# Performance work log

Hardware: AMD Instinct MI355X
Metric: run time of the kernel (lower is better)

## Reference

```python
import jax, jax.numpy as jnp
import numpy as np

BETA = 1.0
NUM_CLASSES = 64  # upper bound on region ids per image (mask.max()+1 in original)


def setup_inputs() -> dict:
    key = jax.random.key(0)
    k1, k2, k3 = jax.random.split(key, 3)
    B, C, H, W = 16, 3, 512, 512
    inp = jax.random.normal(k1, (B, C, H, W), dtype=jnp.float32)
    tgt = jax.random.normal(k2, (B, C, H, W), dtype=jnp.float32)
    mask = jax.random.randint(k3, (B, H, W), 0, NUM_CLASSES, dtype=jnp.int32)
    return {"input": inp, "target": tgt, "mask": mask}


def reference(input, target, mask):
    B, C, H, W = input.shape
    # per-element L1 (reduce=False)
    loss = jnp.abs(input - target)                      # [B,C,H,W]
    w = jax.lax.stop_gradient(loss)                     # detached copy
    # segmented mean over (channels x region pixels) per (batch, class)
    seg = (jnp.arange(B, dtype=mask.dtype)[:, None, None] * NUM_CLASSES + mask).reshape(-1)  # [B*H*W]
    w_csum = w.sum(axis=1).reshape(-1)                  # sum over channels per pixel, [B*H*W]
    sums = jax.ops.segment_sum(w_csum, seg, num_segments=B * NUM_CLASSES)
    cnts = jax.ops.segment_sum(jnp.ones_like(w_csum), seg, num_segments=B * NUM_CLASSES)
    avg = sums / jnp.maximum(cnts * C, 1.0)             # mean over C*area elements; safe for empty regions
    # broadcast region averages back (same value across channels)
    weight = avg[seg].reshape(B, 1, H, W)               # [B,1,H,W]
    weight = weight / jnp.max(weight)
    weight = jnp.clip(weight, 0.0, 1.0)
    return jnp.mean(loss * (weight * BETA + 1.0))
```

## Files before the change

### kernel.cpp

```cpp
#include <hip/hip_runtime.h>
#include <hip/hip_bf16.h>

#define NUM_CLASSES 64
#define BATCH 16
#define CHAN 3
#define HW (512 * 512)
#define BPB 64
#define THREADS 256
#define NREP 4

__global__ __launch_bounds__(THREADS) void frl_accum(
    const float4* __restrict__ inp,
    const float4* __restrict__ tgt,
    const int4* __restrict__ mask,
    float* __restrict__ g_sum,
    unsigned int* __restrict__ g_cnt)
{
    __shared__ float s_sum[NREP][NUM_CLASSES];
    __shared__ unsigned int s_cnt[NREP][NUM_CLASSES];
    const int t = threadIdx.x;
    for (int i = t; i < NREP * NUM_CLASSES; i += THREADS) {
        ((float*)s_sum)[i] = 0.0f;
        ((unsigned int*)s_cnt)[i] = 0u;
    }
    __syncthreads();

    const int b   = blockIdx.x / BPB;
    const int blk = blockIdx.x % BPB;
    const int PPB = HW / BPB;
    const int GPB = PPB / 4;
    const int rep = t & (NREP - 1);

    const int g0    = blk * GPB;
    const int cbase = b * (CHAN * HW / 4);
    const int mbase = b * (HW / 4);

    for (int g = t; g < GPB; g += THREADS) {
        const int4 m4 = mask[mbase + g0 + g];
        float l[4] = {0.f, 0.f, 0.f, 0.f};
        #pragma unroll
        for (int c = 0; c < CHAN; ++c) {
            const int idx = cbase + c * (HW / 4) + g0 + g;
            const float4 a = inp[idx];
            const float4 v = tgt[idx];
            l[0] += fabsf(a.x - v.x);
            l[1] += fabsf(a.y - v.y);
            l[2] += fabsf(a.z - v.z);
            l[3] += fabsf(a.w - v.w);
        }
        atomicAdd(&s_sum[rep][m4.x], l[0]);
        atomicAdd(&s_sum[rep][m4.y], l[1]);
        atomicAdd(&s_sum[rep][m4.z], l[2]);
        atomicAdd(&s_sum[rep][m4.w], l[3]);
        atomicAdd(&s_cnt[rep][m4.x], 1u);
        atomicAdd(&s_cnt[rep][m4.y], 1u);
        atomicAdd(&s_cnt[rep][m4.z], 1u);
        atomicAdd(&s_cnt[rep][m4.w], 1u);
    }
    __syncthreads();
    if (t < NUM_CLASSES) {
        float fs = 0.0f;
        unsigned int cs = 0u;
        #pragma unroll
        for (int r = 0; r < NREP; ++r) { fs += s_sum[r][t]; cs += s_cnt[r][t]; }
        atomicAdd(&g_sum[b * NUM_CLASSES + t], fs);
        atomicAdd(&g_cnt[b * NUM_CLASSES + t], cs);
    }
}

__global__ __launch_bounds__(256) void frl_finalize(
    const float* __restrict__ g_sum,
    const unsigned int* __restrict__ g_cnt,
    float* __restrict__ out)
{
    const int NSEG = BATCH * NUM_CLASSES;
    __shared__ float s_avg[BATCH * NUM_CLASSES];
    __shared__ float red[256];
    const int t = threadIdx.x;

    float lmax = 0.0f;
    for (int s = t; s < NSEG; s += 256) {
        const float sum = g_sum[s];
        const float cnt = (float)g_cnt[s];
        const float avg = sum / fmaxf(cnt * (float)CHAN, 1.0f);
        s_avg[s] = avg;
        lmax = fmaxf(lmax, avg);
    }
    red[t] = lmax;
    __syncthreads();
    for (int off = 128; off > 0; off >>= 1) {
        if (t < off) red[t] = fmaxf(red[t], red[t + off]);
        __syncthreads();
    }
    const float maxavg = fmaxf(red[0], 1e-30f);
    __syncthreads();

    float part = 0.0f;
    for (int s = t; s < NSEG; s += 256) {
        const float w = fminf(fmaxf(s_avg[s] / maxavg, 0.0f), 1.0f);
        part += g_sum[s] * (1.0f + w);
    }
    red[t] = part;
    __syncthreads();
    for (int off = 128; off > 0; off >>= 1) {
        if (t < off) red[t] += red[t + off];
        __syncthreads();
    }
    if (t == 0) {
        out[0] = red[0] / (float)((size_t)BATCH * CHAN * HW);
    }
}

extern "C" void kernel_launch(void* const* d_in, const int* in_sizes, int n_in,
                              void* d_out, int out_size, void* d_ws, size_t ws_size,
                              hipStream_t stream) {
    const float4* inp = (const float4*)d_in[0];
    const float4* tgt = (const float4*)d_in[1];
    const int4* mask  = (const int4*)d_in[2];

    float* g_sum        = (float*)d_ws;
    unsigned int* g_cnt = (unsigned int*)((char*)d_ws + BATCH * NUM_CLASSES * sizeof(float));

    hipMemsetAsync(d_ws, 0, 2 * BATCH * NUM_CLASSES * sizeof(float), stream);
    frl_accum<<<BATCH * BPB, THREADS, 0, stream>>>(inp, tgt, mask, g_sum, g_cnt);
    frl_finalize<<<1, 256, 0, stream>>>(g_sum, g_cnt, (float*)d_out);
}
```

Baseline: 142.9 us.

## Double-buffer global loads in accumulation loop and pad shared histograms

Replaces the strided per-thread loop with a fixed four-iteration unrolled loop that software-prefetches the next iteration's mask, input and target vectors into registers while the current ones are reduced. The first loads are issued before the shared-memory histogram is zeroed, so that latency overlaps the initialisation and barrier. The shared replica arrays get padding to reduce bank conflicts, and launch bounds request two blocks per SM. The aim is to hide memory latency in this bandwidth-bound pass. The cost is higher register pressure, and the fixed NITER assumes GPB equals NITER times THREADS.

```diff
diff --git a/kernel.cpp b/kernel.cpp
--- a/kernel.cpp
+++ b/kernel.cpp
@@ -7,56 +7,86 @@
 #define HW (512 * 512)
 #define BPB 64
 #define THREADS 256
+#define NITER 4
 #define NREP 4
+#define CPAD 8
 
-__global__ __launch_bounds__(THREADS) void frl_accum(
+__global__ __launch_bounds__(THREADS, 2) void frl_accum(
     const float4* __restrict__ inp,
     const float4* __restrict__ tgt,
     const int4* __restrict__ mask,
     float* __restrict__ g_sum,
     unsigned int* __restrict__ g_cnt)
 {
-    __shared__ float s_sum[NREP][NUM_CLASSES];
-    __shared__ unsigned int s_cnt[NREP][NUM_CLASSES];
+    __shared__ float s_sum[NREP][NUM_CLASSES + CPAD];
+    __shared__ unsigned int s_cnt[NREP][NUM_CLASSES + CPAD];
     const int t = threadIdx.x;
-    for (int i = t; i < NREP * NUM_CLASSES; i += THREADS) {
+
+    const int b   = blockIdx.x / BPB;
+    const int blk = blockIdx.x % BPB;
+    const int GPB = HW / 4 / BPB;
+    const int rep = t & (NREP - 1);
+
+    const int g0    = blk * GPB;
+    const int CS    = HW / 4;
+    const int cbase = b * (CHAN * CS) + g0 + t;
+    const int mbase = b * CS + g0 + t;
+
+    int4   ms[2];
+    float4 ai[2][CHAN];
+    float4 at[2][CHAN];
+
+    ms[0]    = mask[mbase];
+    ai[0][0] = inp[cbase + 0 * CS];
+    ai[0][1] = inp[cbase + 1 * CS];
+    ai[0][2] = inp[cbase + 2 * CS];
+    at[0][0] = tgt[cbase + 0 * CS];
+    at[0][1] = tgt[cbase + 1 * CS];
+    at[0][2] = tgt[cbase + 2 * CS];
+
+    for (int i = t; i < NREP * (NUM_CLASSES + CPAD); i += THREADS) {
         ((float*)s_sum)[i] = 0.0f;
         ((unsigned int*)s_cnt)[i] = 0u;
     }
     __syncthreads();
 
-    const int b   = blockIdx.x / BPB;
-    const int blk = blockIdx.x % BPB;
-    const int PPB = HW / BPB;
-    const int GPB = PPB / 4;
-    const int rep = t & (NREP - 1);
+    #pragma unroll
+    for (int it = 0; it < NITER; ++it) {
+        const int cur = it & 1;
+        const int nxt = cur ^ 1;
+        if (it < NITER - 1) {
+            const int off = (it + 1) * THREADS;
+            ms[nxt]    = mask[mbase + off];
+            ai[nxt][0] = inp[cbase + 0 * CS + off];
+            ai[nxt][1] = inp[cbase + 1 * CS + off];
+            ai[nxt][2] = inp[cbase + 2 * CS + off];
+            at[nxt][0] = tgt[cbase + 0 * CS + off];
+            at[nxt][1] = tgt[cbase + 1 * CS + off];
+            at[nxt][2] = tgt[cbase + 2 * CS + off];
+        }
+        const float l0 = fabsf(ai[cur][0].x - at[cur][0].x)
+                       + fabsf(ai[cur][1].x - at[cur][1].x)
+                       + fabsf(ai[cur][2].x - at[cur][2].x);
+        const float l1 = fabsf(ai[cur][0].y - at[cur][0].y)
+                       + fabsf(ai[cur][1].y - at[cur][1].y)
+                       + fabsf(ai[cur][2].y - at[cur][2].y);
+        const float l2 = fabsf(ai[cur][0].z - at[cur][0].z)
+                       + fabsf(ai[cur][1].z - at[cur][1].z)
+                       + fabsf(ai[cur][2].z - at[cur][2].z);
+        const float l3 = fabsf(ai[cur][0].w - at[cur][0].w)
+                       + fabsf(ai[cur][1].w - at[cur][1].w)
+                       + fabsf(ai[cur][2].w - at[cur][2].w);
+        const int4 m = ms[cur];
+        atomicAdd(&s_sum[rep][m.x], l0);
+        atomicAdd(&s_sum[rep][m.y], l1);
+        atomicAdd(&s_sum[rep][m.z], l2);
+        atomicAdd(&s_sum[rep][m.w], l3);
+        atomicAdd(&s_cnt[rep][m.x], 1u);
+        atomicAdd(&s_cnt[rep][m.y], 1u);
+        atomicAdd(&s_cnt[rep][m.z], 1u);
+        atomicAdd(&s_cnt[rep][m.w], 1u);
+    }
 
-    const int g0    = blk * GPB;
-    const int cbase = b * (CHAN * HW / 4);
-    const int mbase = b * (HW / 4);
-
-    for (int g = t; g < GPB; g += THREADS) {
-        const int4 m4 = mask[mbase + g0 + g];
-        float l[4] = {0.f, 0.f, 0.f, 0.f};
-        #pragma unroll
-        for (int c = 0; c < CHAN; ++c) {
-            const int idx = cbase + c * (HW / 4) + g0 + g;
-            const float4 a = inp[idx];
-            const float4 v = tgt[idx];
-            l[0] += fabsf(a.x - v.x);
-            l[1] += fabsf(a.y - v.y);
-            l[2] += fabsf(a.z - v.z);
-            l[3] += fabsf(a.w - v.w);
-        }
-        atomicAdd(&s_sum[rep][m4.x], l[0]);
-        atomicAdd(&s_sum[rep][m4.y], l[1]);
-        atomicAdd(&s_sum[rep][m4.z], l[2]);
-        atomicAdd(&s_sum[rep][m4.w], l[3]);
-        atomicAdd(&s_cnt[rep][m4.x], 1u);
-        atomicAdd(&s_cnt[rep][m4.y], 1u);
-        atomicAdd(&s_cnt[rep][m4.z], 1u);
-        atomicAdd(&s_cnt[rep][m4.w], 1u);
-    }
     __syncthreads();
     if (t < NUM_CLASSES) {
         float fs = 0.0f;
```

Result: no change. 143.0 us (+0.0%).

## Double-buffer inputs via direct global-to-LDS async loads in accumulation kernel

Applied to the files above, without the earlier changes.

Replaces direct per-thread global float4 loads with global_load_lds async copies into a double-buffered LDS staging area per wavefront. The next chunk's loads are issued before the current chunk is processed, using manual vmcnt waits, to overlap memory latency with the compute and atomic work. It also pads the shared histogram arrays. This relies on the 16-byte LDS-direct load support and correct wait counts, and adds LDS usage that may reduce occupancy.

```diff
diff --git a/kernel.cpp b/kernel.cpp
--- a/kernel.cpp
+++ b/kernel.cpp
@@ -7,56 +7,100 @@
 #define HW (512 * 512)
 #define BPB 64
 #define THREADS 256
+#define WAVES 4
+#define PXW 256
+#define CHUNK (PXW * WAVES)
+#define NCHUNK 4
 #define NREP 4
+#define CPAD 8
+#define SLOTS 7
+
+#define WAITCNT_VM7 0xF77
+#define WAITCNT_VM0 0xF70
+
+typedef __attribute__((address_space(3))) void* lds_vp;
+typedef const __attribute__((address_space(1))) void* gm_vp;
 
 __global__ __launch_bounds__(THREADS) void frl_accum(
-    const float4* __restrict__ inp,
-    const float4* __restrict__ tgt,
-    const int4* __restrict__ mask,
+    const float* __restrict__ inp,
+    const float* __restrict__ tgt,
+    const int*   __restrict__ mask,
     float* __restrict__ g_sum,
     unsigned int* __restrict__ g_cnt)
 {
-    __shared__ float s_sum[NREP][NUM_CLASSES];
-    __shared__ unsigned int s_cnt[NREP][NUM_CLASSES];
-    const int t = threadIdx.x;
-    for (int i = t; i < NREP * NUM_CLASSES; i += THREADS) {
+    __shared__ float lds[2][WAVES][SLOTS * PXW];
+    __shared__ float s_sum[NREP][NUM_CLASSES + CPAD];
+    __shared__ unsigned int s_cnt[NREP][NUM_CLASSES + CPAD];
+
+    const int t   = threadIdx.x;
+    const int w   = t >> 6;
+    const int l   = t & 63;
+    const int b   = blockIdx.x / BPB;
+    const int blk = blockIdx.x % BPB;
+    const int rep = t & (NREP - 1);
+
+    const float* inb = inp  + (size_t)b * CHAN * HW;
+    const float* tgb = tgt  + (size_t)b * CHAN * HW;
+    const int*   mkb = mask + (size_t)b * HW;
+
+    auto stage = [&](int buf, int i) {
+        const int px0 = blk * (CHUNK * NCHUNK) + i * CHUNK + w * PXW;
+        float* ldsw = &lds[buf][w][0];
+        #pragma unroll
+        for (int c = 0; c < CHAN; ++c) {
+            __builtin_amdgcn_global_load_lds(
+                (gm_vp)(inb + c * HW + px0 + l * 4),
+                (lds_vp)(ldsw + c * PXW), 16, 0, 0);
+            __builtin_amdgcn_global_load_lds(
+                (gm_vp)(tgb + c * HW + px0 + l * 4),
+                (lds_vp)(ldsw + (3 + c) * PXW), 16, 0, 0);
+        }
+        __builtin_amdgcn_global_load_lds(
+            (gm_vp)(mkb + px0 + l * 4),
+            (lds_vp)(ldsw + 6 * PXW), 16, 0, 0);
+    };
+
+    stage(0, 0);
+
+    for (int i = t; i < NREP * (NUM_CLASSES + CPAD); i += THREADS) {
         ((float*)s_sum)[i] = 0.0f;
         ((unsigned int*)s_cnt)[i] = 0u;
     }
     __syncthreads();
 
-    const int b   = blockIdx.x / BPB;
-    const int blk = blockIdx.x % BPB;
-    const int PPB = HW / BPB;
-    const int GPB = PPB / 4;
-    const int rep = t & (NREP - 1);
+    #pragma unroll
+    for (int i = 0; i < NCHUNK; ++i) {
+        const int buf = i & 1;
+        if (i + 1 < NCHUNK) {
+            stage(buf ^ 1, i + 1);
+            __builtin_amdgcn_s_waitcnt(WAITCNT_VM7);
+        } else {
+            __builtin_amdgcn_s_waitcnt(WAITCNT_VM0);
+        }
+        const float* ldsw = &lds[buf][w][0];
+        const float4 a0 = *(const float4*)(ldsw + 0 * PXW + l * 4);
+        const float4 a1 = *(const float4*)(ldsw + 1 * PXW + l * 4);
+        const float4 a2 = *(const float4*)(ldsw + 2 * PXW + l * 4);
+        const float4 b0 = *(const float4*)(ldsw + 3 * PXW + l * 4);
+        const float4 b1 = *(const float4*)(ldsw + 4 * PXW + l * 4);
+        const float4 b2 = *(const float4*)(ldsw + 5 * PXW + l * 4);
+        const int4   m  = *(const int4*)  (ldsw + 6 * PXW + l * 4);
 
-    const int g0    = blk * GPB;
-    const int cbase = b * (CHAN * HW / 4);
-    const int mbase = b * (HW / 4);
+        const float l0 = fabsf(a0.x - b0.x) + fabsf(a1.x - b1.x) + fabsf(a2.x - b2.x);
+        const float l1 = fabsf(a0.y - b0.y) + fabsf(a1.y - b1.y) + fabsf(a2.y - b2.y);
+        const float l2 = fabsf(a0.z - b0.z) + fabsf(a1.z - b1.z) + fabsf(a2.z - b2.z);
+        const float l3 = fabsf(a0.w - b0.w) + fabsf(a1.w - b1.w) + fabsf(a2.w - b2.w);
 
-    for (int g = t; g < GPB; g += THREADS) {
-        const int4 m4 = mask[mbase + g0 + g];
-        float l[4] = {0.f, 0.f, 0.f, 0.f};
-        #pragma unroll
-        for (int c = 0; c < CHAN; ++c) {
-            const int idx = cbase + c * (HW / 4) + g0 + g;
-            const float4 a = inp[idx];
-            const float4 v = tgt[idx];
-            l[0] += fabsf(a.x - v.x);
-            l[1] += fabsf(a.y - v.y);
-            l[2] += fabsf(a.z - v.z);
-            l[3] += fabsf(a.w - v.w);
-        }
-        atomicAdd(&s_sum[rep][m4.x], l[0]);
-        atomicAdd(&s_sum[rep][m4.y], l[1]);
-        atomicAdd(&s_sum[rep][m4.z], l[2]);
-        atomicAdd(&s_sum[rep][m4.w], l[3]);
-        atomicAdd(&s_cnt[rep][m4.x], 1u);
-        atomicAdd(&s_cnt[rep][m4.y], 1u);
-        atomicAdd(&s_cnt[rep][m4.z], 1u);
-        atomicAdd(&s_cnt[rep][m4.w], 1u);
+        atomicAdd(&s_sum[rep][m.x], l0);
+        atomicAdd(&s_sum[rep][m.y], l1);
+        atomicAdd(&s_sum[rep][m.z], l2);
+        atomicAdd(&s_sum[rep][m.w], l3);
+        atomicAdd(&s_cnt[rep][m.x], 1u);
+        atomicAdd(&s_cnt[rep][m.y], 1u);
+        atomicAdd(&s_cnt[rep][m.z], 1u);
+        atomicAdd(&s_cnt[rep][m.w], 1u);
     }
+
     __syncthreads();
     if (t < NUM_CLASSES) {
         float fs = 0.0f;
@@ -114,9 +158,9 @@
 extern "C" void kernel_launch(void* const* d_in, const int* in_sizes, int n_in,
                               void* d_out, int out_size, void* d_ws, size_t ws_size,
                               hipStream_t stream) {
-    const float4* inp = (const float4*)d_in[0];
-    const float4* tgt = (const float4*)d_in[1];
-    const int4* mask  = (const int4*)d_in[2];
+    const float* inp = (const float*)d_in[0];
+    const float* tgt = (const float*)d_in[1];
+    const int* mask  = (const int*)d_in[2];
 
     float* g_sum        = (float*)d_ws;
     unsigned int* g_cnt = (unsigned int*)((char*)d_ws + BATCH * NUM_CLASSES * sizeof(float));
```

Result: slower. 147.0 us (+2.8%).

## Split accumulation across channels per block with nontemporal loads and full unroll

Applied to the files above, without the earlier changes.

The grid grows from batch×slab blocks to channel×batch×slab blocks. Each block now handles one channel of one slab, and only the channel-0 blocks update the counts. Input and target are read with nontemporal loads, the pixel loop is fully unrolled, and the shared histograms are padded. In exchange, the mask is reread three times, and the shared atomic adds for sums triple because per-pixel channel sums are no longer formed in registers.

```diff
diff --git a/kernel.cpp b/kernel.cpp
--- a/kernel.cpp
+++ b/kernel.cpp
@@ -5,66 +5,72 @@
 #define BATCH 16
 #define CHAN 3
 #define HW (512 * 512)
-#define BPB 64
+#define SLABS 64
+#define SLABPX (HW / SLABS)
 #define THREADS 256
 #define NREP 4
+#define CPAD 8
+
+typedef float  fx4 __attribute__((ext_vector_type(4)));
+typedef int    ix4 __attribute__((ext_vector_type(4)));
 
 __global__ __launch_bounds__(THREADS) void frl_accum(
-    const float4* __restrict__ inp,
-    const float4* __restrict__ tgt,
-    const int4* __restrict__ mask,
+    const fx4* __restrict__ inp,
+    const fx4* __restrict__ tgt,
+    const ix4* __restrict__ mask,
     float* __restrict__ g_sum,
     unsigned int* __restrict__ g_cnt)
 {
-    __shared__ float s_sum[NREP][NUM_CLASSES];
-    __shared__ unsigned int s_cnt[NREP][NUM_CLASSES];
+    __shared__ float s_sum[NREP][NUM_CLASSES + CPAD];
+    __shared__ unsigned int s_cnt[NREP][NUM_CLASSES + CPAD];
     const int t = threadIdx.x;
-    for (int i = t; i < NREP * NUM_CLASSES; i += THREADS) {
+    for (int i = t; i < NREP * (NUM_CLASSES + CPAD); i += THREADS) {
         ((float*)s_sum)[i] = 0.0f;
         ((unsigned int*)s_cnt)[i] = 0u;
     }
     __syncthreads();
 
-    const int b   = blockIdx.x / BPB;
-    const int blk = blockIdx.x % BPB;
-    const int PPB = HW / BPB;
-    const int GPB = PPB / 4;
-    const int rep = t & (NREP - 1);
+    const int slab = blockIdx.x & 63;
+    const int b    = (blockIdx.x >> 6) & 15;
+    const int c    = blockIdx.x >> 10;
+    const int rep  = t & (NREP - 1);
 
-    const int g0    = blk * GPB;
-    const int cbase = b * (CHAN * HW / 4);
-    const int mbase = b * (HW / 4);
+    const int G     = SLABPX / 4;
+    const int dbase = (b * CHAN + c) * (HW / 4) + slab * G;
+    const int mbase = b * (HW / 4) + slab * G;
+    const bool count = (c == 0);
 
-    for (int g = t; g < GPB; g += THREADS) {
-        const int4 m4 = mask[mbase + g0 + g];
-        float l[4] = {0.f, 0.f, 0.f, 0.f};
-        #pragma unroll
-        for (int c = 0; c < CHAN; ++c) {
-            const int idx = cbase + c * (HW / 4) + g0 + g;
-            const float4 a = inp[idx];
-            const float4 v = tgt[idx];
-            l[0] += fabsf(a.x - v.x);
-            l[1] += fabsf(a.y - v.y);
-            l[2] += fabsf(a.z - v.z);
-            l[3] += fabsf(a.w - v.w);
+    #pragma unroll
+    for (int i = 0; i < G / THREADS; ++i) {
+        const int g = i * THREADS + t;
+        const fx4 a = __builtin_nontemporal_load(&inp[dbase + g]);
+        const fx4 v = __builtin_nontemporal_load(&tgt[dbase + g]);
+        const ix4 m = mask[mbase + g];
+
+        atomicAdd(&s_sum[rep][m.x], fabsf(a.x - v.x));
+        atomicAdd(&s_sum[rep][m.y], fabsf(a.y - v.y));
+        atomicAdd(&s_sum[rep][m.z], fabsf(a.z - v.z));
+        atomicAdd(&s_sum[rep][m.w], fabsf(a.w - v.w));
+        if (count) {
+            atomicAdd(&s_cnt[rep][m.x], 1u);
+            atomicAdd(&s_cnt[rep][m.y], 1u);
+            atomicAdd(&s_cnt[rep][m.z], 1u);
+            atomicAdd(&s_cnt[rep][m.w], 1u);
         }
-        atomicAdd(&s_sum[rep][m4.x], l[0]);
-        atomicAdd(&s_sum[rep][m4.y], l[1]);
-        atomicAdd(&s_sum[rep][m4.z], l[2]);
-        atomicAdd(&s_sum[rep][m4.w], l[3]);
-        atomicAdd(&s_cnt[rep][m4.x], 1u);
-        atomicAdd(&s_cnt[rep][m4.y], 1u);
-        atomicAdd(&s_cnt[rep][m4.z], 1u);
-        atomicAdd(&s_cnt[rep][m4.w], 1u);
     }
+
     __syncthreads();
     if (t < NUM_CLASSES) {
         float fs = 0.0f;
-        unsigned int cs = 0u;
         #pragma unroll
-        for (int r = 0; r < NREP; ++r) { fs += s_sum[r][t]; cs += s_cnt[r][t]; }
+        for (int r = 0; r < NREP; ++r) fs += s_sum[r][t];
         atomicAdd(&g_sum[b * NUM_CLASSES + t], fs);
-        atomicAdd(&g_cnt[b * NUM_CLASSES + t], cs);
+        if (count) {
+            unsigned int cs = 0u;
+            #pragma unroll
+            for (int r = 0; r < NREP; ++r) cs += s_cnt[r][t];
+            atomicAdd(&g_cnt[b * NUM_CLASSES + t], cs);
+        }
     }
 }
 
@@ -114,14 +120,14 @@
 extern "C" void kernel_launch(void* const* d_in, const int* in_sizes, int n_in,
                               void* d_out, int out_size, void* d_ws, size_t ws_size,
                               hipStream_t stream) {
-    const float4* inp = (const float4*)d_in[0];
-    const float4* tgt = (const float4*)d_in[1];
-    const int4* mask  = (const int4*)d_in[2];
+    const fx4* inp = (const fx4*)d_in[0];
+    const fx4* tgt = (const fx4*)d_in[1];
+    const ix4* mask = (const ix4*)d_in[2];
 
     float* g_sum        = (float*)d_ws;
     unsigned int* g_cnt = (unsigned int*)((char*)d_ws + BATCH * NUM_CLASSES * sizeof(float));
 
-    hipMemsetAsync(d_ws, 0, 2 * BATCH * NUM_CLASSES * sizeof(float), stream);
-    frl_accum<<<BATCH * BPB, THREADS, 0, stream>>>(inp, tgt, mask, g_sum, g_cnt);
+    (void)hipMemsetAsync(d_ws, 0, 2 * BATCH * NUM_CLASSES * sizeof(float), stream);
+    frl_accum<<<CHAN * BATCH * SLABS, THREADS, 0, stream>>>(inp, tgt, mask, g_sum, g_cnt);
     frl_finalize<<<1, 256, 0, stream>>>(g_sum, g_cnt, (float*)d_out);
 }
```

After: 183.9 us. +28.7%, slower.
